# Kernel tuning notes

Hardware: AMD Instinct MI355X
Metric: run time of the kernel (lower is better)

Reference implementation:

```python
import jax, jax.numpy as jnp
import numpy as np

N_NODES = 100000
N_EDGES = 1_600_000
D_IN = 128
D_OUT = 128


def setup_inputs() -> dict:
    key = jax.random.key(0)
    k_x, k_w, k_col, k_row = jax.random.split(key, 4)
    X = jax.random.normal(k_x, (N_NODES, D_IN), dtype=jnp.float32)
    weights = jax.random.normal(k_w, (D_IN, D_OUT), dtype=jnp.float32) * (1.0 / np.sqrt(D_OUT))
    # edge list: destination rows sorted (CSR order), random source columns
    edgeToRow = jnp.sort(jax.random.randint(k_row, (N_EDGES,), 0, N_NODES, dtype=jnp.int32))
    column_index = jax.random.randint(k_col, (N_EDGES,), 0, N_NODES, dtype=jnp.int32)
    # row_pointers consistent with edgeToRow
    row_np = np.asarray(edgeToRow)
    row_pointers = jnp.asarray(np.searchsorted(row_np, np.arange(N_NODES + 1)), dtype=jnp.int32)
    # TC-GNN-style tiling metadata (layout only; does not affect math)
    n_windows = (N_NODES + 15) // 16
    blockPartition = jnp.ones((n_windows,), dtype=jnp.int32)
    edgeToColumn = jnp.zeros((N_EDGES,), dtype=jnp.int32)
    hybrid_type = jnp.zeros((n_windows,), dtype=jnp.int32)
    row_nzr = jnp.zeros((n_windows + 1,), dtype=jnp.int32)
    col_nzr = jnp.zeros((N_NODES,), dtype=jnp.int32)
    return {
        "X": X,
        "weights": weights,
        "row_pointers": row_pointers,
        "column_index": column_index,
        "blockPartition": blockPartition,
        "edgeToColumn": edgeToColumn,
        "edgeToRow": edgeToRow,
        "hybrid_type": hybrid_type,
        "row_nzr": row_nzr,
        "col_nzr": col_nzr,
    }


def reference(X, weights, row_pointers, column_index, blockPartition,
              edgeToColumn, edgeToRow, hybrid_type, row_nzr, col_nzr):
    # Fused SpMM aggregation (A @ X with implicit unit edge values) + dense GEMM.
    # blockPartition/edgeToColumn/hybrid_type/row_nzr/col_nzr are kernel layout
    # metadata and do not change the math.
    gathered = jnp.take(X, column_index, axis=0)                  # [E, D_IN]
    X_prime = jax.ops.segment_sum(gathered, edgeToRow,
                                  num_segments=X.shape[0])        # [N, D_IN]
    return X_prime @ weights                                      # [N, D_OUT]
```

## Files before the change

### kernel.cpp

```cpp
#include <hip/hip_runtime.h>
#include <hip/hip_bf16.h>

typedef short short8 __attribute__((ext_vector_type(8)));
typedef float floatx4 __attribute__((ext_vector_type(4)));

__device__ __forceinline__ unsigned short f2bf_u(float f) {
    __hip_bfloat16 h = __float2bfloat16(f);
    return *reinterpret_cast<unsigned short*>(&h);
}

__device__ __forceinline__ void acc2(float2& acc, unsigned u) {
    unsigned lo = u << 16;
    unsigned hi = u & 0xffff0000u;
    acc.x += __builtin_bit_cast(float, lo);
    acc.y += __builtin_bit_cast(float, hi);
}

__global__ void wprep_kernel(const float* __restrict__ W,
                             __hip_bfloat16* __restrict__ Wt) {
    int tid = blockIdx.x * blockDim.x + threadIdx.x;
    int n = tid & 127;
    int k = tid >> 7;
    Wt[n * 128 + k] = __float2bfloat16(W[k * 128 + n]);
}

__global__ __launch_bounds__(256)
void gemm_kernel(const float* __restrict__ X,
                 const __hip_bfloat16* __restrict__ Wt,
                 char* __restrict__ Yb) {
    __shared__ unsigned short As[32 * 128];

    int tid = threadIdx.x;
    size_t rowbase = (size_t)blockIdx.x * 32;

    {
        int rr = tid >> 5;
        int c4 = (tid & 31) * 4;
        int kb = c4 >> 3;
        int ko = c4 & 7;
#pragma unroll
        for (int it = 0; it < 4; ++it) {
            int row = it * 8 + rr;
            float4 f = *(const float4*)(X + (rowbase + row) * 128 + c4);
            uint2 p;
            p.x = (unsigned)f2bf_u(f.x) | ((unsigned)f2bf_u(f.y) << 16);
            p.y = (unsigned)f2bf_u(f.z) | ((unsigned)f2bf_u(f.w) << 16);
            *(uint2*)(As + row * 128 + ((kb ^ (row & 15)) << 3) + ko) = p;
        }
    }
    __syncthreads();

    int wv   = tid >> 6;
    int lane = tid & 63;
    int m16  = lane & 15;
    int quad = lane >> 4;
    int rt   = wv & 1;
    int ctb  = (wv >> 1) * 4;

    floatx4 acc[4] = {{0,0,0,0},{0,0,0,0},{0,0,0,0},{0,0,0,0}};
    int arow = rt * 16 + m16;
#pragma unroll
    for (int s = 0; s < 4; ++s) {
        int kb = quad + s * 4;
        short8 bfrag = *(const short8*)(As + arow * 128 + ((kb ^ m16) << 3));
#pragma unroll
        for (int t = 0; t < 4; ++t) {
            short8 afrag = *(const short8*)(Wt + ((ctb + t) * 16 + m16) * 128 +
                                            quad * 8 + s * 32);
            acc[t] = __builtin_amdgcn_mfma_f32_16x16x32_bf16(afrag, bfrag,
                                                             acc[t], 0, 0, 0);
        }
    }

    size_t orow = rowbase + rt * 16 + m16;
#pragma unroll
    for (int t = 0; t < 4; ++t) {
        int ocol = (ctb + t) * 16 + quad * 4;
        uint2 p;
        p.x = (unsigned)f2bf_u(acc[t][0]) | ((unsigned)f2bf_u(acc[t][1]) << 16);
        p.y = (unsigned)f2bf_u(acc[t][2]) | ((unsigned)f2bf_u(acc[t][3]) << 16);
        *(uint2*)(Yb + orow * 256 + ocol * 2) = p;
    }
}

__global__ __launch_bounds__(256)
void agg_kernel(const char* __restrict__ Yb,
                const int* __restrict__ row_pointers,
                const int* __restrict__ column_index,
                float* __restrict__ out) {
    int lane = threadIdx.x & 63;
    int r    = blockIdx.x * 4 + (threadIdx.x >> 6);
    int sub  = lane >> 5;
    int fg   = lane & 31;
    int foff = fg * 8;

    int e0 = row_pointers[r];
    int e1 = row_pointers[r + 1];

    float2 a0 = {0.f, 0.f}, a1 = {0.f, 0.f};

    int e = e0;
    int efull = e0 + ((e1 - e0) & ~7);
    for (; e < efull; e += 8) {
        int c0 = column_index[e + sub];
        int c1 = column_index[e + 2 + sub];
        int c2 = column_index[e + 4 + sub];
        int c3 = column_index[e + 6 + sub];
        uint2 u0 = *(const uint2*)(Yb + (size_t)c0 * 256 + foff);
        uint2 u1 = *(const uint2*)(Yb + (size_t)c1 * 256 + foff);
        uint2 u2 = *(const uint2*)(Yb + (size_t)c2 * 256 + foff);
        uint2 u3 = *(const uint2*)(Yb + (size_t)c3 * 256 + foff);
        acc2(a0, u0.x); acc2(a1, u0.y);
        acc2(a0, u1.x); acc2(a1, u1.y);
        acc2(a0, u2.x); acc2(a1, u2.y);
        acc2(a0, u3.x); acc2(a1, u3.y);
    }
    for (; e < e1; e += 2) {
        int idx   = e + sub;
        bool valid = idx < e1;
        int c = column_index[valid ? idx : e1 - 1];
        uint2 u = *(const uint2*)(Yb + (size_t)c * 256 + foff);
        if (!valid) { u.x = 0u; u.y = 0u; }
        acc2(a0, u.x); acc2(a1, u.y);
    }

    a0.x += __shfl_xor(a0.x, 32);
    a0.y += __shfl_xor(a0.y, 32);
    a1.x += __shfl_xor(a1.x, 32);
    a1.y += __shfl_xor(a1.y, 32);

    if (sub == 0) {
        float4 v = {a0.x, a0.y, a1.x, a1.y};
        *(float4*)(out + (size_t)r * 128 + fg * 4) = v;
    }
}

extern "C" void kernel_launch(void* const* d_in, const int* in_sizes, int n_in,
                              void* d_out, int out_size, void* d_ws, size_t ws_size,
                              hipStream_t stream) {
    const float* X       = (const float*)d_in[0];
    const float* W       = (const float*)d_in[1];
    const int* row_ptrs  = (const int*)d_in[2];
    const int* col_index = (const int*)d_in[3];

    float* out = (float*)d_out;
    const int N = in_sizes[2] - 1;

    char* ws = (char*)d_ws;
    __hip_bfloat16* Wt = (__hip_bfloat16*)ws;
    char* Yb = ws + 32768;

    wprep_kernel<<<64, 256, 0, stream>>>(W, Wt);
    gemm_kernel<<<N / 32, 256, 0, stream>>>(X, Wt, Yb);
    agg_kernel<<<N / 4, 256, 0, stream>>>(Yb, row_ptrs, col_index, out);
}
```

Before: 214.4 us.

## Widen aggregation gathers to 16-byte loads with four edges per wave step

The aggregation kernel now gives each lane 8 bf16 features (a 16-byte load) instead of 4. A wave handles 4 edges at a time instead of 2, and 16 edges per unrolled iteration. This cuts the number of load instructions per gathered row and keeps more edges in flight, but adds an extra shuffle stage for the reduction and a larger partial tail. The X loads in the GEMM and the output stores now use nontemporal hints to avoid polluting the cache.

```diff
diff --git a/kernel.cpp b/kernel.cpp
--- a/kernel.cpp
+++ b/kernel.cpp
@@ -3,17 +3,27 @@
 
 typedef short short8 __attribute__((ext_vector_type(8)));
 typedef float floatx4 __attribute__((ext_vector_type(4)));
+typedef unsigned int uintx4 __attribute__((ext_vector_type(4)));
+typedef unsigned int uintx2 __attribute__((ext_vector_type(2)));
 
 __device__ __forceinline__ unsigned short f2bf_u(float f) {
     __hip_bfloat16 h = __float2bfloat16(f);
     return *reinterpret_cast<unsigned short*>(&h);
 }
 
-__device__ __forceinline__ void acc2(float2& acc, unsigned u) {
-    unsigned lo = u << 16;
-    unsigned hi = u & 0xffff0000u;
-    acc.x += __builtin_bit_cast(float, lo);
-    acc.y += __builtin_bit_cast(float, hi);
+__device__ __forceinline__ float bflo(unsigned u) {
+    unsigned l = u << 16;
+    return __builtin_bit_cast(float, l);
+}
+__device__ __forceinline__ float bfhi(unsigned u) {
+    unsigned h = u & 0xffff0000u;
+    return __builtin_bit_cast(float, h);
+}
+__device__ __forceinline__ void acc_u4(floatx4& A, floatx4& B, uintx4 u) {
+    A.x += bflo(u.x); A.y += bfhi(u.x);
+    A.z += bflo(u.y); A.w += bfhi(u.y);
+    B.x += bflo(u.z); B.y += bfhi(u.z);
+    B.z += bflo(u.w); B.w += bfhi(u.w);
 }
 
 __global__ void wprep_kernel(const float* __restrict__ W,
@@ -41,11 +51,12 @@
 #pragma unroll
         for (int it = 0; it < 4; ++it) {
             int row = it * 8 + rr;
-            float4 f = *(const float4*)(X + (rowbase + row) * 128 + c4);
-            uint2 p;
+            floatx4 f = __builtin_nontemporal_load(
+                (const floatx4*)(X + (rowbase + row) * 128 + c4));
+            uintx2 p;
             p.x = (unsigned)f2bf_u(f.x) | ((unsigned)f2bf_u(f.y) << 16);
             p.y = (unsigned)f2bf_u(f.z) | ((unsigned)f2bf_u(f.w) << 16);
-            *(uint2*)(As + row * 128 + ((kb ^ (row & 15)) << 3) + ko) = p;
+            *(uintx2*)(As + row * 128 + ((kb ^ (row & 15)) << 3) + ko) = p;
         }
     }
     __syncthreads();
@@ -76,10 +87,10 @@
 #pragma unroll
     for (int t = 0; t < 4; ++t) {
         int ocol = (ctb + t) * 16 + quad * 4;
-        uint2 p;
+        uintx2 p;
         p.x = (unsigned)f2bf_u(acc[t][0]) | ((unsigned)f2bf_u(acc[t][1]) << 16);
         p.y = (unsigned)f2bf_u(acc[t][2]) | ((unsigned)f2bf_u(acc[t][3]) << 16);
-        *(uint2*)(Yb + orow * 256 + ocol * 2) = p;
+        *(uintx2*)(Yb + orow * 256 + ocol * 2) = p;
     }
 }
 
@@ -88,50 +99,62 @@
                 const int* __restrict__ row_pointers,
                 const int* __restrict__ column_index,
                 float* __restrict__ out) {
-    int lane = threadIdx.x & 63;
-    int r    = blockIdx.x * 4 + (threadIdx.x >> 6);
-    int sub  = lane >> 5;
-    int fg   = lane & 31;
-    int foff = fg * 8;
+    int tid  = threadIdx.x;
+    int lane = tid & 63;
+    int r    = blockIdx.x * 4 + (tid >> 6);
+    int sub  = lane >> 4;
+    int fo   = (lane & 15) * 16;
 
     int e0 = row_pointers[r];
     int e1 = row_pointers[r + 1];
 
-    float2 a0 = {0.f, 0.f}, a1 = {0.f, 0.f};
+    floatx4 accA = {0.f, 0.f, 0.f, 0.f};
+    floatx4 accB = {0.f, 0.f, 0.f, 0.f};
 
     int e = e0;
-    int efull = e0 + ((e1 - e0) & ~7);
-    for (; e < efull; e += 8) {
+    int elast = e0 + ((e1 - e0) & ~15);
+    for (; e < elast; e += 16) {
         int c0 = column_index[e + sub];
-        int c1 = column_index[e + 2 + sub];
-        int c2 = column_index[e + 4 + sub];
-        int c3 = column_index[e + 6 + sub];
-        uint2 u0 = *(const uint2*)(Yb + (size_t)c0 * 256 + foff);
-        uint2 u1 = *(const uint2*)(Yb + (size_t)c1 * 256 + foff);
-        uint2 u2 = *(const uint2*)(Yb + (size_t)c2 * 256 + foff);
-        uint2 u3 = *(const uint2*)(Yb + (size_t)c3 * 256 + foff);
-        acc2(a0, u0.x); acc2(a1, u0.y);
-        acc2(a0, u1.x); acc2(a1, u1.y);
-        acc2(a0, u2.x); acc2(a1, u2.y);
-        acc2(a0, u3.x); acc2(a1, u3.y);
+        int c1 = column_index[e + 4 + sub];
+        int c2 = column_index[e + 8 + sub];
+        int c3 = column_index[e + 12 + sub];
+        uintx4 u0 = *(const uintx4*)(Yb + (size_t)c0 * 256 + fo);
+        uintx4 u1 = *(const uintx4*)(Yb + (size_t)c1 * 256 + fo);
+        uintx4 u2 = *(const uintx4*)(Yb + (size_t)c2 * 256 + fo);
+        uintx4 u3 = *(const uintx4*)(Yb + (size_t)c3 * 256 + fo);
+        acc_u4(accA, accB, u0);
+        acc_u4(accA, accB, u1);
+        acc_u4(accA, accB, u2);
+        acc_u4(accA, accB, u3);
     }
-    for (; e < e1; e += 2) {
-        int idx   = e + sub;
-        bool valid = idx < e1;
-        int c = column_index[valid ? idx : e1 - 1];
-        uint2 u = *(const uint2*)(Yb + (size_t)c * 256 + foff);
-        if (!valid) { u.x = 0u; u.y = 0u; }
-        acc2(a0, u.x); acc2(a1, u.y);
+    if (e < e1) {
+#pragma unroll
+        for (int g = 0; g < 4; ++g) {
+            int idx = e + g * 4 + sub;
+            if (idx < e1) {
+                int c = column_index[idx];
+                uintx4 u = *(const uintx4*)(Yb + (size_t)c * 256 + fo);
+                acc_u4(accA, accB, u);
+            }
+        }
     }
 
-    a0.x += __shfl_xor(a0.x, 32);
-    a0.y += __shfl_xor(a0.y, 32);
-    a1.x += __shfl_xor(a1.x, 32);
-    a1.y += __shfl_xor(a1.y, 32);
+#pragma unroll
+    for (int m = 16; m <= 32; m <<= 1) {
+        accA.x += __shfl_xor(accA.x, m);
+        accA.y += __shfl_xor(accA.y, m);
+        accA.z += __shfl_xor(accA.z, m);
+        accA.w += __shfl_xor(accA.w, m);
+        accB.x += __shfl_xor(accB.x, m);
+        accB.y += __shfl_xor(accB.y, m);
+        accB.z += __shfl_xor(accB.z, m);
+        accB.w += __shfl_xor(accB.w, m);
+    }
 
     if (sub == 0) {
-        float4 v = {a0.x, a0.y, a1.x, a1.y};
-        *(float4*)(out + (size_t)r * 128 + fg * 4) = v;
+        float* dst = out + (size_t)r * 128 + (lane & 15) * 8;
+        __builtin_nontemporal_store(accA, (floatx4*)dst);
+        __builtin_nontemporal_store(accB, (floatx4*)(dst + 4));
     }
 }
 
```

After: 209.9 us. 1.02x faster.
